# Kernel optimization log

Hardware: AMD Instinct MI355X
Metric: run time of the kernel (lower is better)

## Reference

```python
import jax, jax.numpy as jnp
import numpy as np

# Earth4D config (matches init_kwargs)
L_SPATIAL = 16
L_TEMPORAL = 16
FEAT = 2
LOG2_T = 19
TABLE = 1 << LOG2_T            # 524288 entries per level (power of 2)
BASE_S = 32.0
BASE_T = 32.0
GROWTH = 2.0
N_PTS = 131072

_CORNERS = np.array([[i, j, k] for i in (0, 1) for j in (0, 1) for k in (0, 1)], dtype=np.int32)  # [8,3]


def _encode3d(x, tables, base, growth):
    """Multi-resolution hash-grid encoding (torch-ngp / instant-ngp math).
    x: [N,3] in [0,1]; tables: [L, TABLE, FEAT]. Returns [N, L*FEAT]."""
    L, T, F = tables.shape
    corners = jnp.asarray(_CORNERS)  # [8,3]
    outs = []
    for l in range(L):  # static loop over levels (L=16)
        res = int(np.floor(base * growth ** l))
        pos = x * res                      # [N,3]
        pos_floor = jnp.floor(pos)
        w = pos - pos_floor                # fractional part, [N,3]
        base_idx = pos_floor.astype(jnp.int32)
        c = base_idx[:, None, :] + corners[None]   # [N,8,3] corner grid coords
        if (res + 1) ** 3 <= T:
            # coarse level: dense (stride) indexing, no collisions
            s = res + 1
            idx = c[..., 0] + c[..., 1] * s + c[..., 2] * s * s  # [N,8]
        else:
            # fine level: spatial hash with instant-ngp primes
            cu = c.astype(jnp.uint32)
            h = (cu[..., 0] * jnp.uint32(1)) ^ (cu[..., 1] * jnp.uint32(2654435761)) ^ (cu[..., 2] * jnp.uint32(805459861))
            idx = (h & jnp.uint32(T - 1)).astype(jnp.int32)      # [N,8]
        feats = tables[l][idx]             # gather, [N,8,F]
        # trilinear weights: prod over dims of (w if corner==1 else 1-w)
        wts = jnp.prod(jnp.where(corners[None] == 1, w[:, None, :], 1.0 - w[:, None, :]), axis=-1)  # [N,8]
        outs.append(jnp.einsum('ncf,nc->nf', feats, wts.astype(feats.dtype)))
    return jnp.concatenate(outs, axis=-1)  # [N, L*F]


def setup_inputs() -> dict:
    key = jax.random.key(0)
    k0, k1, k2, k3, k4 = jax.random.split(key, 5)
    xyzt = jax.random.uniform(k0, (N_PTS, 4), dtype=jnp.float32)  # normalized coords in [0,1]
    init = lambda k, L: jax.random.uniform(k, (L, TABLE, FEAT), dtype=jnp.float32, minval=-1e-4, maxval=1e-4)
    return {
        'xyzt': xyzt,
        'spatial_tables': init(k1, L_SPATIAL),
        'xyt_tables': init(k2, L_TEMPORAL),
        'yzt_tables': init(k3, L_TEMPORAL),
        'xzt_tables': init(k4, L_TEMPORAL),
    }


def reference(xyzt, spatial_tables, xyt_tables, yzt_tables, xzt_tables):
    x, y, z, t = xyzt[:, 0], xyzt[:, 1], xyzt[:, 2], xyzt[:, 3]
    xyz = xyzt[:, :3]
    xyt = jnp.stack([x, y, t], axis=-1)
    yzt = jnp.stack([y, z, t], axis=-1)
    xzt = jnp.stack([x, z, t], axis=-1)
    f_xyz = _encode3d(xyz, spatial_tables, BASE_S, GROWTH)   # [N, 32]
    f_xyt = _encode3d(xyt, xyt_tables, BASE_T, GROWTH)       # [N, 32]
    f_yzt = _encode3d(yzt, yzt_tables, BASE_T, GROWTH)       # [N, 32]
    f_xzt = _encode3d(xzt, xzt_tables, BASE_T, GROWTH)       # [N, 32]
    return jnp.concatenate([f_xyz, f_xyt, f_yzt, f_xzt], axis=-1)  # [N, 128]
```

## Files before the change

kernel.cpp:

```cpp
#include <hip/hip_runtime.h>

#define N_PTS 131072
#define LOG2_T 19
#define TABLE_SIZE (1u << LOG2_T)
#define HASH_MASK (TABLE_SIZE - 1u)

typedef float f32x2 __attribute__((ext_vector_type(2)));
typedef float f32x4 __attribute__((ext_vector_type(4)));

template <bool USE_WS>
__global__ __launch_bounds__(256, 2) void earth4d_gather(
    const float* __restrict__ xyzt,
    const float* __restrict__ tab_xyz,
    const float* __restrict__ tab_xyt,
    const float* __restrict__ tab_yzt,
    const float* __restrict__ tab_xzt,
    float* __restrict__ out,
    f32x2* __restrict__ ws)
{
    unsigned b     = blockIdx.x;
    unsigned xcd   = b & 7u;
    unsigned i     = b >> 3;
    unsigned combo = ((i >> 7) << 3) | xcd;
    unsigned chunk = i & 127u;
    unsigned e     = combo >> 4;
    unsigned l     = combo & 15u;

    const float* tab;
    switch (e) {
      case 0:  tab = tab_xyz; break;
      case 1:  tab = tab_xyt; break;
      case 2:  tab = tab_yzt; break;
      default: tab = tab_xzt; break;
    }
    const f32x2* tl = reinterpret_cast<const f32x2*>(tab) + (size_t)l * TABLE_SIZE;

    unsigned resu = 32u << l;
    float res = (float)resu;

    unsigned nbase = (chunk << 10) | threadIdx.x;

    float w0[4], w1[4], w2[4];
    unsigned idx[4][8];

    #pragma unroll
    for (int k = 0; k < 4; ++k) {
        unsigned n = nbase + (unsigned)k * 256u;
        float4 p = reinterpret_cast<const float4*>(xyzt)[n];
        float c0, c1, c2;
        switch (e) {
          case 0:  c0 = p.x; c1 = p.y; c2 = p.z; break;
          case 1:  c0 = p.x; c1 = p.y; c2 = p.w; break;
          case 2:  c0 = p.y; c1 = p.z; c2 = p.w; break;
          default: c0 = p.x; c1 = p.z; c2 = p.w; break;
        }
        float p0 = c0 * res, p1 = c1 * res, p2 = c2 * res;
        float f0 = floorf(p0), f1 = floorf(p1), f2 = floorf(p2);
        w0[k] = p0 - f0; w1[k] = p1 - f1; w2[k] = p2 - f2;
        int b0 = (int)f0, b1 = (int)f1, b2 = (int)f2;

        if (l < 2u) {
            int s = (int)resu + 1;
            #pragma unroll
            for (int c = 0; c < 8; ++c) {
                int i0 = b0 + ((c >> 2) & 1);
                int i1 = b1 + ((c >> 1) & 1);
                int i2 = b2 + (c & 1);
                idx[k][c] = (unsigned)(i0 + i1 * s + i2 * s * s);
            }
        } else {
            #pragma unroll
            for (int c = 0; c < 8; ++c) {
                unsigned i0 = (unsigned)(b0 + ((c >> 2) & 1));
                unsigned i1 = (unsigned)(b1 + ((c >> 1) & 1));
                unsigned i2 = (unsigned)(b2 + (c & 1));
                idx[k][c] = (i0 * 1u ^ i1 * 2654435761u ^ i2 * 805459861u) & HASH_MASK;
            }
        }
    }

    f32x2 v[4][8];
    #pragma unroll
    for (int k = 0; k < 4; ++k)
        #pragma unroll
        for (int c = 0; c < 8; ++c)
            v[k][c] = tl[idx[k][c]];

    #pragma unroll
    for (int k = 0; k < 4; ++k) {
        float a0 = 0.f, a1 = 0.f;
        #pragma unroll
        for (int c = 0; c < 8; ++c) {
            float wt = ((c & 4) ? w0[k] : 1.f - w0[k])
                     * ((c & 2) ? w1[k] : 1.f - w1[k])
                     * ((c & 1) ? w2[k] : 1.f - w2[k]);
            a0 = fmaf(v[k][c].x, wt, a0);
            a1 = fmaf(v[k][c].y, wt, a1);
        }
        unsigned n = nbase + (unsigned)k * 256u;
        f32x2 r = { a0, a1 };
        if (USE_WS) {
            __builtin_nontemporal_store(r, ws + (size_t)combo * N_PTS + n);
        } else {
            __builtin_nontemporal_store(
                r, reinterpret_cast<f32x2*>(out + (size_t)n * 128u + combo * 2u));
        }
    }
}

__global__ __launch_bounds__(256) void earth4d_transpose(
    const f32x2* __restrict__ ws, float* __restrict__ out)
{
    __shared__ f32x2 lds[64][65];
    unsigned n0 = blockIdx.x * 64u;
    unsigned t = threadIdx.x;

    #pragma unroll
    for (int it = 0; it < 16; ++it) {
        unsigned i = (unsigned)it * 256u + t;
        unsigned c = i >> 6;
        unsigned p = i & 63u;
        lds[p][c] = __builtin_nontemporal_load(ws + (size_t)c * N_PTS + n0 + p);
    }
    __syncthreads();

    #pragma unroll
    for (int it = 0; it < 8; ++it) {
        unsigned i = (unsigned)it * 256u + t;
        unsigned p = i >> 5;
        unsigned q = i & 31u;
        f32x2 a = lds[p][2u * q];
        f32x2 b = lds[p][2u * q + 1u];
        f32x4 v = { a.x, a.y, b.x, b.y };
        __builtin_nontemporal_store(
            v, reinterpret_cast<f32x4*>(out + (size_t)(n0 + p) * 128u) + q);
    }
}

extern "C" void kernel_launch(void* const* d_in, const int* in_sizes, int n_in,
                              void* d_out, int out_size, void* d_ws, size_t ws_size,
                              hipStream_t stream) {
    const float* xyzt    = (const float*)d_in[0];
    const float* tab_xyz = (const float*)d_in[1];
    const float* tab_xyt = (const float*)d_in[2];
    const float* tab_yzt = (const float*)d_in[3];
    const float* tab_xzt = (const float*)d_in[4];
    float* out = (float*)d_out;

    const size_t ws_needed = (size_t)64 * N_PTS * sizeof(f32x2);
    dim3 grid1(8192u), block(256u);

    if (ws_size >= ws_needed && d_ws) {
        f32x2* ws = (f32x2*)d_ws;
        earth4d_gather<true><<<grid1, block, 0, stream>>>(
            xyzt, tab_xyz, tab_xyt, tab_yzt, tab_xzt, out, ws);
        earth4d_transpose<<<dim3(N_PTS / 64u), block, 0, stream>>>(ws, out);
    } else {
        earth4d_gather<false><<<grid1, block, 0, stream>>>(
            xyzt, tab_xyz, tab_xyt, tab_yzt, tab_xzt, out, (f32x2*)nullptr);
    }
}
```

Measured before the change: 345.3 us.

## Convert hash tables to scaled fp16 before the gather to halve gather bytes

Adds a pre-pass kernel that converts all four fp32 hash tables to fp16, scaled by 512 to keep the small values in normal range, and writes them into workspace. The gather then fetches 4-byte fp16 pairs instead of 8-byte fp32 pairs and rescales the accumulated result. The goal is to halve the table footprint so random gathers hit cache more often. In exchange, every call must read the full fp32 tables and write the fp16 copy, adds a launch, needs more workspace, and loses some precision.

```diff
diff --git a/kernel.cpp b/kernel.cpp
--- a/kernel.cpp
+++ b/kernel.cpp
@@ -7,16 +7,40 @@
 
 typedef float f32x2 __attribute__((ext_vector_type(2)));
 typedef float f32x4 __attribute__((ext_vector_type(4)));
-
-template <bool USE_WS>
+typedef _Float16 h16x2 __attribute__((ext_vector_type(2)));
+typedef _Float16 h16x4 __attribute__((ext_vector_type(4)));
+
+#define FSCALE 512.0f
+#define INV_FSCALE (1.0f / 512.0f)
+
+__global__ __launch_bounds__(256) void earth4d_convert(
+    const float* __restrict__ t0, const float* __restrict__ t1,
+    const float* __restrict__ t2, const float* __restrict__ t3,
+    h16x4* __restrict__ dst)
+{
+    const float* srcs[4] = {t0, t1, t2, t3};
+    unsigned tid = blockIdx.x * 256u + threadIdx.x;
+    #pragma unroll
+    for (int it = 0; it < 8; ++it) {
+        unsigned q = tid + (unsigned)it * 2097152u;
+        const f32x4* src = reinterpret_cast<const f32x4*>(srcs[q >> 22]);
+        f32x4 v = __builtin_nontemporal_load(src + (q & 0x3FFFFFu));
+        h16x4 h = { (_Float16)(v.x * FSCALE), (_Float16)(v.y * FSCALE),
+                    (_Float16)(v.z * FSCALE), (_Float16)(v.w * FSCALE) };
+        dst[q] = h;
+    }
+}
+
+template <int MODE>
 __global__ __launch_bounds__(256, 2) void earth4d_gather(
     const float* __restrict__ xyzt,
     const float* __restrict__ tab_xyz,
     const float* __restrict__ tab_xyt,
     const float* __restrict__ tab_yzt,
     const float* __restrict__ tab_xzt,
+    const h16x2* __restrict__ tab16,
     float* __restrict__ out,
-    f32x2* __restrict__ ws)
+    f32x2* __restrict__ stage)
 {
     unsigned b     = blockIdx.x;
     unsigned xcd   = b & 7u;
@@ -33,7 +57,8 @@
       case 2:  tab = tab_yzt; break;
       default: tab = tab_xzt; break;
     }
-    const f32x2* tl = reinterpret_cast<const f32x2*>(tab) + (size_t)l * TABLE_SIZE;
+    const f32x2* tl32 = reinterpret_cast<const f32x2*>(tab) + (size_t)l * TABLE_SIZE;
+    const h16x2* tl16 = tab16 + (size_t)combo * TABLE_SIZE;
 
     unsigned resu = 32u << l;
     float res = (float)resu;
@@ -79,28 +104,57 @@
         }
     }
 
-    f32x2 v[4][8];
-    #pragma unroll
-    for (int k = 0; k < 4; ++k)
-        #pragma unroll
-        for (int c = 0; c < 8; ++c)
-            v[k][c] = tl[idx[k][c]];
+    float r0[4], r1[4];
+    if (MODE == 0) {
+        h16x2 v[4][8];
+        #pragma unroll
+        for (int k = 0; k < 4; ++k)
+            #pragma unroll
+            for (int c = 0; c < 8; ++c)
+                v[k][c] = tl16[idx[k][c]];
+        #pragma unroll
+        for (int k = 0; k < 4; ++k) {
+            float a0 = 0.f, a1 = 0.f;
+            #pragma unroll
+            for (int c = 0; c < 8; ++c) {
+                float wt = ((c & 4) ? w0[k] : 1.f - w0[k])
+                         * ((c & 2) ? w1[k] : 1.f - w1[k])
+                         * ((c & 1) ? w2[k] : 1.f - w2[k]);
+                a0 = fmaf((float)v[k][c].x, wt, a0);
+                a1 = fmaf((float)v[k][c].y, wt, a1);
+            }
+            r0[k] = a0 * INV_FSCALE;
+            r1[k] = a1 * INV_FSCALE;
+        }
+    } else {
+        f32x2 v[4][8];
+        #pragma unroll
+        for (int k = 0; k < 4; ++k)
+            #pragma unroll
+            for (int c = 0; c < 8; ++c)
+                v[k][c] = tl32[idx[k][c]];
+        #pragma unroll
+        for (int k = 0; k < 4; ++k) {
+            float a0 = 0.f, a1 = 0.f;
+            #pragma unroll
+            for (int c = 0; c < 8; ++c) {
+                float wt = ((c & 4) ? w0[k] : 1.f - w0[k])
+                         * ((c & 2) ? w1[k] : 1.f - w1[k])
+                         * ((c & 1) ? w2[k] : 1.f - w2[k]);
+                a0 = fmaf(v[k][c].x, wt, a0);
+                a1 = fmaf(v[k][c].y, wt, a1);
+            }
+            r0[k] = a0;
+            r1[k] = a1;
+        }
+    }
 
     #pragma unroll
     for (int k = 0; k < 4; ++k) {
-        float a0 = 0.f, a1 = 0.f;
-        #pragma unroll
-        for (int c = 0; c < 8; ++c) {
-            float wt = ((c & 4) ? w0[k] : 1.f - w0[k])
-                     * ((c & 2) ? w1[k] : 1.f - w1[k])
-                     * ((c & 1) ? w2[k] : 1.f - w2[k]);
-            a0 = fmaf(v[k][c].x, wt, a0);
-            a1 = fmaf(v[k][c].y, wt, a1);
-        }
         unsigned n = nbase + (unsigned)k * 256u;
-        f32x2 r = { a0, a1 };
-        if (USE_WS) {
-            __builtin_nontemporal_store(r, ws + (size_t)combo * N_PTS + n);
+        f32x2 r = { r0[k], r1[k] };
+        if (MODE != 2) {
+            __builtin_nontemporal_store(r, stage + (size_t)combo * N_PTS + n);
         } else {
             __builtin_nontemporal_store(
                 r, reinterpret_cast<f32x2*>(out + (size_t)n * 128u + combo * 2u));
@@ -147,16 +201,25 @@
     const float* tab_xzt = (const float*)d_in[4];
     float* out = (float*)d_out;
 
-    const size_t ws_needed = (size_t)64 * N_PTS * sizeof(f32x2);
-    dim3 grid1(8192u), block(256u);
-
-    if (ws_size >= ws_needed && d_ws) {
-        f32x2* ws = (f32x2*)d_ws;
-        earth4d_gather<true><<<grid1, block, 0, stream>>>(
-            xyzt, tab_xyz, tab_xyt, tab_yzt, tab_xzt, out, ws);
-        earth4d_transpose<<<dim3(N_PTS / 64u), block, 0, stream>>>(ws, out);
+    const size_t TAB16 = (size_t)64 * TABLE_SIZE * sizeof(h16x2);
+    const size_t STAGE = (size_t)64 * N_PTS * sizeof(f32x2);
+    dim3 block(256u), grid1(8192u);
+
+    if (d_ws && ws_size >= TAB16 + STAGE) {
+        h16x2* tab16 = (h16x2*)d_ws;
+        f32x2* stage = (f32x2*)((char*)d_ws + TAB16);
+        earth4d_convert<<<dim3(8192u), block, 0, stream>>>(
+            tab_xyz, tab_xyt, tab_yzt, tab_xzt, (h16x4*)tab16);
+        earth4d_gather<0><<<grid1, block, 0, stream>>>(
+            xyzt, tab_xyz, tab_xyt, tab_yzt, tab_xzt, tab16, out, stage);
+        earth4d_transpose<<<dim3(N_PTS / 64u), block, 0, stream>>>(stage, out);
+    } else if (d_ws && ws_size >= STAGE) {
+        f32x2* stage = (f32x2*)d_ws;
+        earth4d_gather<1><<<grid1, block, 0, stream>>>(
+            xyzt, tab_xyz, tab_xyt, tab_yzt, tab_xzt, (const h16x2*)nullptr, out, stage);
+        earth4d_transpose<<<dim3(N_PTS / 64u), block, 0, stream>>>(stage, out);
     } else {
-        earth4d_gather<false><<<grid1, block, 0, stream>>>(
-            xyzt, tab_xyz, tab_xyt, tab_yzt, tab_xzt, out, (f32x2*)nullptr);
-    }
-}
+        earth4d_gather<2><<<grid1, block, 0, stream>>>(
+            xyzt, tab_xyz, tab_xyt, tab_yzt, tab_xzt, (const h16x2*)nullptr, out, (f32x2*)nullptr);
+    }
+}
```

Result: slower. 358.5 us (+3.8%).
